# Kernel tuning notes

Measured on AMD Instinct MI355X. Metric: run time of the kernel, lower is better.

Reference implementation:

```python
import math
import jax, jax.numpy as jnp
import numpy as np
from jax import lax

# ---- static config (mirrors RPN init + typical torchvision anchor setup) ----
IMG_H = IMG_W = 800
LEVELS = [(200, 200, 4, 32), (100, 100, 8, 64), (50, 50, 16, 128), (25, 25, 32, 256), (13, 13, 64, 512)]  # (h, w, stride, anchor_size)
RATIOS = (0.5, 1.0, 2.0)
COUNTS = tuple(h * w * len(RATIOS) for (h, w, _, _) in LEVELS)  # (120000,30000,7500,1875,507)
A_TOTAL = sum(COUNTS)  # 159882
PRE_NMS = 2000
POST_NMS = 1000
NMS_THRESH = 0.7
MIN_SIZE = 1e-3
BBOX_CLIP = math.log(1000.0 / 16)


def make_anchors():
    parts = []
    for (h, w, stride, size) in LEVELS:
        ws = np.array([size * np.sqrt(1.0 / r) for r in RATIOS], np.float32)  # [3]
        hs = np.array([size * np.sqrt(r) for r in RATIOS], np.float32)
        sx = (np.arange(w, dtype=np.float32) + 0.5) * stride
        sy = (np.arange(h, dtype=np.float32) + 0.5) * stride
        cy, cx = np.meshgrid(sy, sx, indexing='ij')
        cx = cx.reshape(-1, 1)
        cy = cy.reshape(-1, 1)
        a = np.stack([cx - ws / 2, cy - hs / 2, cx + ws / 2, cy + hs / 2], axis=-1)  # [HW,3,4]
        parts.append(a.reshape(-1, 4))
    return np.concatenate(parts, 0).astype(np.float32)


def setup_inputs() -> dict:
    key = jax.random.key(0)
    k1, k2 = jax.random.split(key)
    scores = jax.random.normal(k1, (1, A_TOTAL), dtype=jnp.float32)
    deltas = jax.random.normal(k2, (A_TOTAL, 4), dtype=jnp.float32) * 0.5
    anchors = jnp.asarray(make_anchors())
    return {'scores': scores, 'deltas': deltas, 'anchors': anchors}


def _pairwise_iou(b):
    area = (b[:, 2] - b[:, 0]) * (b[:, 3] - b[:, 1])  # [K]
    lt = jnp.maximum(b[:, None, :2], b[None, :, :2])   # [K,K,2]
    rb = jnp.minimum(b[:, None, 2:], b[None, :, 2:])
    wh = jnp.maximum(rb - lt, 0.0)
    inter = wh[..., 0] * wh[..., 1]
    return inter / (area[:, None] + area[None, :] - inter)


def reference(scores, deltas, anchors):
    s_all = lax.stop_gradient(scores[0])  # original does cls.detach()
    # ---- box decode (torchvision-style) ----
    w = anchors[:, 2] - anchors[:, 0]
    h = anchors[:, 3] - anchors[:, 1]
    cx = anchors[:, 0] + 0.5 * w
    cy = anchors[:, 1] + 0.5 * h
    dx, dy = deltas[:, 0], deltas[:, 1]
    dw = jnp.minimum(deltas[:, 2], BBOX_CLIP)
    dh = jnp.minimum(deltas[:, 3], BBOX_CLIP)
    px = cx + dx * w
    py = cy + dy * h
    pw = jnp.exp(dw) * w
    ph = jnp.exp(dh) * h
    boxes = jnp.stack([px - 0.5 * pw, py - 0.5 * ph, px + 0.5 * pw, py + 0.5 * ph], axis=1)  # [A,4]
    # ---- per-level top-k over objectness ----
    idx_parts = []
    off = 0
    for c in COUNTS:
        k = min(PRE_NMS, c)
        _, ti = lax.top_k(lax.dynamic_slice_in_dim(s_all, off, c), k)
        idx_parts.append(ti + off)
        off += c
    top_idx = jnp.concatenate(idx_parts)  # [K=8382]
    K = top_idx.shape[0]
    s = s_all[top_idx]
    b = boxes[top_idx]
    # ---- clip to image + min-size validity (masked instead of compacted) ----
    b = jnp.stack([jnp.clip(b[:, 0], 0.0, IMG_W), jnp.clip(b[:, 1], 0.0, IMG_H),
                   jnp.clip(b[:, 2], 0.0, IMG_W), jnp.clip(b[:, 3], 0.0, IMG_H)], axis=1)
    valid = ((b[:, 2] - b[:, 0]) >= MIN_SIZE) & ((b[:, 3] - b[:, 1]) >= MIN_SIZE)
    # ---- per-level NMS offset; replicates original feature_mask[keep] indexing
    # (positional indexing into the full anchor-order level-id vector) ----
    fmask_full = np.concatenate([np.full(c, i, np.float32) for i, c in enumerate(COUNTS)])
    fmask = jnp.asarray(fmask_full[:K])
    box_max = jnp.max(jnp.where(valid[:, None], b, -jnp.inf))
    bn = b + (fmask * (box_max + 1.0))[:, None]
    # ---- greedy NMS on score-sorted candidates ----
    s_m = jnp.where(valid, s, -jnp.inf)
    order = jnp.argsort(-s_m)
    s_srt = s_m[order]
    b_srt = b[order]
    iou = _pairwise_iou(bn[order])  # [K,K] ~281MB
    ar = jnp.arange(K)

    def body(i, keep):
        sup = (iou[i] > NMS_THRESH) & (ar > i)
        return jnp.where(keep[i], keep & ~sup, keep)

    keep = lax.fori_loop(0, K, body, s_srt > -jnp.inf)
    final = jnp.where(keep, s_srt, -jnp.inf)
    out_s, oidx = lax.top_k(final, POST_NMS)  # top post_nms kept, score order; -inf pads
    out_b = b_srt[oidx]
    return out_b, out_s
```

## Files before the change

### kernel.cpp

```cpp
#include <hip/hip_runtime.h>
#include <math.h>

typedef unsigned int u32;
typedef unsigned long long u64;
typedef unsigned char u8;

#define K_TOT 8382
#define NCH 131
#define CAP 1024
#define EC 64
#define GCAP 32768
#define IMGSZ 800.0f

__device__ __constant__ int LOFF[5] = {0, 120000, 150000, 157500, 159375};
__device__ __constant__ int LCNT[5] = {120000, 30000, 7500, 1875, 507};
__device__ __constant__ int KSEL[5] = {2000, 2000, 2000, 1875, 507};
__device__ __constant__ int SELB[5] = {0, 2000, 4000, 6000, 7875};
__device__ __constant__ int HBS[4] = {0, 118, 148, 156};
__device__ __constant__ int GBS[6] = {0, 118, 148, 156, 158, 159};

static __device__ __forceinline__ u32 fkey(float x) {
    u32 u = __float_as_uint(x);
    u32 m = (u32)(((int)u) >> 31) | 0x80000000u;
    return u ^ m;
}

static __device__ __forceinline__ int lvl_of(int s) {
    return (s < 2000) ? 0 : (s < 4000) ? 1 : (s < 6000) ? 2 : (s < 7875) ? 3 : 4;
}

static __device__ __forceinline__ u32 rdl32(u32 v, int j) {
    return (u32)__builtin_amdgcn_readlane((int)v, j);
}
static __device__ __forceinline__ u64 rdlane64(u64 v, int j) {
    u32 lo = (u32)__builtin_amdgcn_readlane((int)(u32)v, j);
    u32 hi = (u32)__builtin_amdgcn_readlane((int)(u32)(v >> 32), j);
    return ((u64)hi << 32) | (u64)lo;
}

static __device__ __forceinline__ u32 wor32(u32 x) {
    x |= (u32)__builtin_amdgcn_update_dpp(0, (int)x, 0x111, 0xf, 0xf, true);
    x |= (u32)__builtin_amdgcn_update_dpp(0, (int)x, 0x112, 0xf, 0xf, true);
    x |= (u32)__builtin_amdgcn_update_dpp(0, (int)x, 0x114, 0xf, 0xf, true);
    x |= (u32)__builtin_amdgcn_update_dpp(0, (int)x, 0x118, 0xf, 0xf, true);
    x |= (u32)__builtin_amdgcn_update_dpp(0, (int)x, 0x142, 0xa, 0xf, true);
    x |= (u32)__builtin_amdgcn_update_dpp(0, (int)x, 0x143, 0xc, 0xf, true);
    return x;
}

static __device__ __forceinline__ void thresh_scan(const u32* hist, u32* scanbuf, int m,
                                                   u32 need, u32* sv, int t) {
    for (int i = t; i < m; i += 1024) scanbuf[i] = hist[m - 1 - i];
    __syncthreads();
    for (int ofs = 1; ofs < m; ofs <<= 1) {
        int i0 = t, i1 = t + 1024;
        u32 a0 = 0, a1 = 0;
        if (i0 < m && i0 >= ofs) a0 = scanbuf[i0 - ofs];
        if (i1 < m && i1 >= ofs) a1 = scanbuf[i1 - ofs];
        __syncthreads();
        if (i0 < m && i0 >= ofs) scanbuf[i0] += a0;
        if (i1 < m && i1 >= ofs) scanbuf[i1] += a1;
        __syncthreads();
    }
    for (int i = t; i < m; i += 1024) {
        u32 inc = scanbuf[i];
        u32 exc = i ? scanbuf[i - 1] : 0;
        if (inc >= need && exc < need) { sv[0] = (u32)(m - 1 - i); sv[1] = need - exc; }
    }
    __syncthreads();
}

__global__ __launch_bounds__(1024) void k_hist(const float* __restrict__ scores,
                                               u32* __restrict__ hist3) {
    __shared__ u32 lh[2048];
    int t = threadIdx.x;
    lh[t] = 0; lh[t + 1024] = 0;
    __syncthreads();
    int b = blockIdx.x;
    int l = (b < HBS[1]) ? 0 : (b < HBS[2]) ? 1 : 2;
    int i = (b - HBS[l]) * 1024 + t;
    if (i < LCNT[l]) atomicAdd(&lh[fkey(scores[LOFF[l] + i]) >> 21], 1u);
    __syncthreads();
    u32* h = hist3 + l * 2048;
    if (lh[t]) atomicAdd(&h[t], lh[t]);
    if (lh[t + 1024]) atomicAdd(&h[t + 1024], lh[t + 1024]);
}

__global__ __launch_bounds__(1024) void k_thresh(const u32* __restrict__ hist3,
                                                 u32* __restrict__ tinfo) {
    __shared__ u32 scanbuf[2048];
    __shared__ u32 sv[2];
    int l = blockIdx.x;
    int t = threadIdx.x;
    thresh_scan(hist3 + l * 2048, scanbuf, 2048, (u32)KSEL[l], sv, t);
    if (t == 0) { tinfo[l * 2] = sv[0]; tinfo[l * 2 + 1] = sv[1]; }
}

__global__ __launch_bounds__(1024) void k_gather(const float* __restrict__ scores,
                                                 const u32* __restrict__ tinfo,
                                                 u32* __restrict__ sel, u32* __restrict__ cgt,
                                                 u32* __restrict__ gcnt, u32* __restrict__ gidx,
                                                 u32* __restrict__ gkey) {
    int b = blockIdx.x;
    int l = (b < GBS[1]) ? 0 : (b < GBS[2]) ? 1 : (b < GBS[3]) ? 2 : (b < GBS[4]) ? 3 : 4;
    int i = (b - GBS[l]) * 1024 + threadIdx.x;
    if (i >= LCNT[l]) return;
    int off = LOFF[l], sb = SELB[l];
    if (l >= 3) { sel[sb + i] = (u32)(off + i); return; }
    u32 ky = fkey(scores[off + i]);
    u32 b1 = tinfo[l * 2];
    u32 top = ky >> 21;
    if (top > b1) {
        u32 p = atomicAdd(&cgt[l], 1u);
        sel[sb + p] = (u32)(off + i);
    } else if (top == b1) {
        u32 e = atomicAdd(&gcnt[l], 1u);
        if (e < GCAP) { gidx[l * GCAP + e] = (u32)i; gkey[l * GCAP + e] = ky; }
    }
}

__global__ __launch_bounds__(1024) void k_final(const u32* __restrict__ gidx,
                                                const u32* __restrict__ gkey,
                                                const u32* __restrict__ gcnt,
                                                const u32* __restrict__ tinfo,
                                                u32* __restrict__ sel) {
    __shared__ u32 hist[2048];
    __shared__ u32 scanbuf[2048];
    __shared__ u32 eqbuf[1024];
    __shared__ u32 sv[2];
    __shared__ u32 c2, ceq;
    int l = blockIdx.x;
    int t = threadIdx.x;
    int k = KSEL[l], sb = SELB[l], off = LOFF[l];
    u32 m = gcnt[l]; if (m > GCAP) m = GCAP;
    u32 b1 = tinfo[l * 2];
    u32 need = tinfo[l * 2 + 1];
    const u32* kb = gkey + l * GCAP;
    const u32* ib = gidx + l * GCAP;
    hist[t] = 0; hist[t + 1024] = 0; __syncthreads();
    for (u32 e = t; e < m; e += 1024) atomicAdd(&hist[(kb[e] >> 10) & 2047u], 1u);
    __syncthreads();
    thresh_scan(hist, scanbuf, 2048, need, sv, t);
    u32 b2 = sv[0], need2 = sv[1];
    __syncthreads();
    hist[t] = 0; __syncthreads();
    for (u32 e = t; e < m; e += 1024) {
        u32 ky = kb[e];
        if (((ky >> 10) & 2047u) == b2) atomicAdd(&hist[ky & 1023u], 1u);
    }
    __syncthreads();
    thresh_scan(hist, scanbuf, 1024, need2, sv, t);
    u32 T = (b1 << 21) | (b2 << 10) | sv[0];
    u32 take = sv[1];
    if (t == 0) { c2 = 0; ceq = 0; }
    __syncthreads();
    u32 nGTbin = need - take;
    u32 base2 = (u32)sb + (u32)k - need;
    for (u32 e = t; e < m; e += 1024) {
        u32 ky = kb[e];
        if (ky > T) { u32 p = atomicAdd(&c2, 1u); sel[base2 + p] = (u32)off + ib[e]; }
        else if (ky == T) { u32 q = atomicAdd(&ceq, 1u); if (q < 1024) eqbuf[q] = ib[e]; }
    }
    __syncthreads();
    if (t == 0) {
        int n = (ceq > 1024u) ? 1024 : (int)ceq;
        for (int a = 1; a < n; ++a) {
            u32 v = eqbuf[a]; int bq = a - 1;
            while (bq >= 0 && eqbuf[bq] > v) { eqbuf[bq + 1] = eqbuf[bq]; --bq; }
            eqbuf[bq + 1] = v;
        }
        for (u32 q = 0; q < take; ++q) sel[base2 + nGTbin + q] = (u32)off + eqbuf[q];
    }
}

__global__ void k_decode(const float* __restrict__ scores, const float4* __restrict__ deltas,
                         const float4* __restrict__ anchors, const u32* __restrict__ sel,
                         float4* __restrict__ candB, float* __restrict__ candS,
                         u32* __restrict__ candV, u32* __restrict__ candA) {
    int s = blockIdx.x * 256 + threadIdx.x;
    if (s >= K_TOT) return;
    u32 a = sel[s];
    float4 an = anchors[a];
    float4 dl = deltas[a];
    float sc = scores[a];
    float w = __fsub_rn(an.z, an.x), h = __fsub_rn(an.w, an.y);
    float cx = __fadd_rn(an.x, __fmul_rn(0.5f, w));
    float cy = __fadd_rn(an.y, __fmul_rn(0.5f, h));
    const float CLIPV = (float)4.1351665567423563;
    float dw = fminf(dl.z, CLIPV);
    float dh = fminf(dl.w, CLIPV);
    float px = __fadd_rn(cx, __fmul_rn(dl.x, w));
    float py = __fadd_rn(cy, __fmul_rn(dl.y, h));
    float pw = __fmul_rn((float)exp((double)dw), w);
    float ph = __fmul_rn((float)exp((double)dh), h);
    float x1 = __fsub_rn(px, __fmul_rn(0.5f, pw));
    float y1 = __fsub_rn(py, __fmul_rn(0.5f, ph));
    float x2 = __fadd_rn(px, __fmul_rn(0.5f, pw));
    float y2 = __fadd_rn(py, __fmul_rn(0.5f, ph));
    x1 = fminf(fmaxf(x1, 0.0f), IMGSZ);
    y1 = fminf(fmaxf(y1, 0.0f), IMGSZ);
    x2 = fminf(fmaxf(x2, 0.0f), IMGSZ);
    y2 = fminf(fmaxf(y2, 0.0f), IMGSZ);
    bool valid = (__fsub_rn(x2, x1) >= 0.001f) && (__fsub_rn(y2, y1) >= 0.001f);
    candB[s] = make_float4(x1, y1, x2, y2);
    candS[s] = sc;
    candV[s] = valid ? 1u : 0u;
    candA[s] = a;
}

__global__ __launch_bounds__(256) void k_rank_lvl(const float* __restrict__ candS,
                                                  const u32* __restrict__ candA,
                                                  u32* __restrict__ Praw) {
    __shared__ u64 tile[256];
    int l = blockIdx.z;
    int cnt = KSEL[l], base = SELB[l];
    int tx = blockIdx.x * 256;
    int ty = blockIdx.y * 256;
    if (tx >= cnt || ty >= cnt) return;
    int t = threadIdx.x;
    u64 Aj = ~0ull;
    if (tx + t < cnt) {
        int j = base + tx + t;
        Aj = ((u64)(~fkey(candS[j])) << 32) | (u64)candA[j];
    }
    tile[t] = Aj;
    __syncthreads();
    int si = ty + t;
    if (si >= cnt) return;
    int s = base + si;
    u64 A = ((u64)(~fkey(candS[s])) << 32) | (u64)candA[s];
    int r = 0;
#pragma unroll 8
    for (int q = 0; q < 256; ++q) r += (tile[q] < A);
    if (r) atomicAdd(&Praw[s], (u32)r);
}

__global__ __launch_bounds__(256) void k_rank_glob(const float* __restrict__ candS,
                                                   const u32* __restrict__ candV,
                                                   const u32* __restrict__ Praw,
                                                   u32* __restrict__ rank) {
    __shared__ u64 colB[256];
    int t = threadIdx.x;
    int cj = blockIdx.x * 256 + t;
    u64 B = ~0ull;
    if (cj < K_TOT) {
        u32 smk = candV[cj] ? fkey(candS[cj]) : 0x007FFFFFu;
        u32 Pj = (u32)SELB[lvl_of(cj)] + Praw[cj];
        B = ((u64)(~smk) << 32) | (u64)Pj;
    }
    colB[t] = B;
    __syncthreads();
    int s = blockIdx.y * 256 + t;
    if (s >= K_TOT) return;
    u32 smk = candV[s] ? fkey(candS[s]) : 0x007FFFFFu;
    u32 Ps = (u32)SELB[lvl_of(s)] + Praw[s];
    u64 myB = ((u64)(~smk) << 32) | (u64)Ps;
    int cnt = 0;
#pragma unroll 8
    for (int j = 0; j < 256; ++j) cnt += (colB[j] < myB);
    if (cnt) atomicAdd(&rank[s], (u32)cnt);
}

__global__ void k_scatter(const float4* __restrict__ candB, const float* __restrict__ candS,
                          const u32* __restrict__ candV, const u32* __restrict__ rank,
                          float4* __restrict__ sB, float* __restrict__ sArea,
                          float* __restrict__ sS, u32* __restrict__ sV) {
    int s = blockIdx.x * 256 + threadIdx.x;
    if (s >= K_TOT) return;
    u32 r = rank[s];
    float4 b = candB[s];
    float area = __fmul_rn(__fsub_rn(b.z, b.x), __fsub_rn(b.w, b.y));
    sB[r] = b; sArea[r] = area; sS[r] = candS[s]; sV[r] = candV[s];
}

__global__ __launch_bounds__(256) void k_mask(const float4* __restrict__ sB,
                                              const float* __restrict__ sArea,
                                              const u32* __restrict__ sV,
                                              u64* __restrict__ vwords,
                                              u64* __restrict__ diag, u32* __restrict__ ecnt,
                                              ulonglong2* __restrict__ epack,
                                              u64* __restrict__ dmask) {
    __shared__ float4 cb[64];
    __shared__ float ca[64];
    int wd = blockIdx.x;
    int t = threadIdx.x;
    if (t < 64) {
        int j = wd * 64 + t;
        if (j < K_TOT) { cb[t] = sB[j]; ca[t] = sArea[j]; }
        else { cb[t] = make_float4(0.f, 0.f, 0.f, 0.f); ca[t] = 0.f; }
    }
    __syncthreads();
    int i = blockIdx.y * 256 + t;
    if (i >= K_TOT) return;
    int dwr = i >> 6;
    if (wd < dwr) return;
    float4 bi = sB[i];
    float ai = sArea[i];
    u64 bits = 0;
    int jbase = wd * 64;
    for (int j2 = 0; j2 < 64; ++j2) {
        int j = jbase + j2;
        if (j > i && j < K_TOT) {
            float4 bj = cb[j2];
            float ltx = fmaxf(bi.x, bj.x), lty = fmaxf(bi.y, bj.y);
            float rbx = fminf(bi.z, bj.z), rby = fminf(bi.w, bj.w);
            float wx = fmaxf(__fsub_rn(rbx, ltx), 0.0f);
            float wy = fmaxf(__fsub_rn(rby, lty), 0.0f);
            float inter = __fmul_rn(wx, wy);
            if (inter > 0.0f) {
                float uni = __fsub_rn(__fadd_rn(ai, ca[j2]), inter);
                float iou = inter / uni;
                if (iou > 0.7f) bits |= (1ull << j2);
            }
        }
    }
    if (wd == dwr) {
        diag[i] = bits;
        u64 vb = __ballot(sV[i] != 0u);
        u64 db = __ballot(bits != 0ull);
        if ((i & 63) == 0) { vwords[wd] = vb; dmask[wd] = db; }
    } else if (bits != 0ull) {
        u32 p = atomicAdd(&ecnt[wd], 1u);
        if (p < CAP) epack[wd * CAP + p] = make_ulonglong2((u64)i, bits);
    }
}

__global__ __launch_bounds__(1024) void k_scan(const u64* __restrict__ diag,
                                               const u64* __restrict__ vwords,
                                               const u32* __restrict__ ecnt,
                                               const ulonglong2* __restrict__ tpack,
                                               const u64* __restrict__ dmask,
                                               const float4* __restrict__ sB,
                                               const float* __restrict__ sS,
                                               float* __restrict__ out) {
    __shared__ ulonglong2 sTpack[NCH * EC];
    __shared__ u64 sKeepArr[NCH];
    __shared__ u32 pc[NCH + 1];
    int t = threadIdx.x;
    int w = t >> 6, lane = t & 63;
    {
        int e0 = t, e1 = t + 1024, e2 = t + 2048, e3 = t + 3072, e4 = t + 4096;
        int e5 = t + 5120, e6 = t + 6144, e7 = t + 7168, e8 = t + 8192;
        bool p8 = e8 < NCH * EC;
        ulonglong2 a0 = tpack[(size_t)(e0 >> 6) * CAP + (e0 & 63)];
        ulonglong2 a1 = tpack[(size_t)(e1 >> 6) * CAP + (e1 & 63)];
        ulonglong2 a2 = tpack[(size_t)(e2 >> 6) * CAP + (e2 & 63)];
        ulonglong2 a3 = tpack[(size_t)(e3 >> 6) * CAP + (e3 & 63)];
        ulonglong2 a4 = tpack[(size_t)(e4 >> 6) * CAP + (e4 & 63)];
        ulonglong2 a5 = tpack[(size_t)(e5 >> 6) * CAP + (e5 & 63)];
        ulonglong2 a6 = tpack[(size_t)(e6 >> 6) * CAP + (e6 & 63)];
        ulonglong2 a7 = tpack[(size_t)(e7 >> 6) * CAP + (e7 & 63)];
        ulonglong2 a8 = make_ulonglong2(0ull, 0ull);
        if (p8) a8 = tpack[(size_t)(e8 >> 6) * CAP + (e8 & 63)];
        sTpack[e0] = a0; sTpack[e1] = a1; sTpack[e2] = a2; sTpack[e3] = a3;
        sTpack[e4] = a4; sTpack[e5] = a5; sTpack[e6] = a6; sTpack[e7] = a7;
        if (p8) sTpack[e8] = a8;
    }
    u64 v0 = 0, v1 = 0, v2 = 0, m0 = 0, m1 = 0, m2 = 0;
    u32 c0 = 0, c1 = 0, c2 = 0;
    if (w == 0) {
        int i0 = lane, i1 = lane + 64, i2 = lane + 128;
        bool p2 = (i2 < NCH);
        v0 = vwords[i0]; v1 = vwords[i1]; v2 = p2 ? vwords[i2] : 0;
        c0 = ecnt[i0]; c1 = ecnt[i1]; c2 = p2 ? ecnt[i2] : 0;
        m0 = dmask[i0]; m1 = dmask[i1]; m2 = p2 ? dmask[i2] : 0;
        if (c0 > CAP) c0 = CAP;
        if (c1 > CAP) c1 = CAP;
        if (c2 > CAP) c2 = CAP;
    }
    __syncthreads();
    if (w == 0) {
        ulonglong2 Ea = sTpack[EC + lane];
        u64 Dcur = diag[lane];
        u64 Dnx  = diag[64 + lane];
        u64 vw = rdlane64(v0, 0), dmw = rdlane64(m0, 0);
        u64 inc = 0;
        u32 cntn = rdl32(c0, 1);
        for (int c = 0; c < NCH; ++c) {
            int cn  = (c + 1 < NCH) ? (c + 1) : c;
            int cn2 = (c + 2 < NCH) ? (c + 2) : c;
            ulonglong2 Eb = sTpack[cn2 * EC + lane];
            u64 Dnn = diag[cn2 * 64 + lane];
            u32 sidx = (u32)Ea.x;
            u32 sch = sidx >> 6;
            u64 Kw = sKeepArr[(sch < (u32)NCH) ? sch : 0];
            u32 cntn2; u64 vwn, dmn;
            if (cn < 64)       { vwn = rdlane64(v0, cn);       dmn = rdlane64(m0, cn); }
            else if (cn < 128) { vwn = rdlane64(v1, cn - 64);  dmn = rdlane64(m1, cn - 64); }
            else               { vwn = rdlane64(v2, cn - 128); dmn = rdlane64(m2, cn - 128); }
            if (cn2 < 64)       cntn2 = rdl32(c0, cn2);
            else if (cn2 < 128) cntn2 = rdl32(c1, cn2 - 64);
            else                cntn2 = rdl32(c2, cn2 - 128);
            u64 alive = vw & ~inc;
            if (dmw) {
                u64 dm = dmw & alive;
                while (dm) {
                    int j = __builtin_ctzll(dm);
                    dm &= dm - 1;
                    if ((alive >> j) & 1ull) {
                        alive &= ~rdlane64(Dcur, j);
                        dm &= alive;
                    }
                }
            }
            if (lane == 0) sKeepArr[c] = alive;
            u64 m = 0;
            if ((u32)lane < cntn) {
                u64 kw2 = (sch == (u32)c) ? alive : Kw;
                if ((kw2 >> (sidx & 63u)) & 1ull) m = Ea.y;
            }
            u32 lo = wor32((u32)m);
            u32 hi = wor32((u32)(m >> 32));
            u64 incn = ((u64)rdl32(hi, 63) << 32) | (u64)rdl32(lo, 63);
            if (cntn > (u32)EC) {
                u64 mt = 0;
                for (u32 e = (u32)EC + (u32)lane; e < cntn; e += 64u) {
                    ulonglong2 Et = tpack[(size_t)cn * CAP + e];
                    u32 si = (u32)Et.x;
                    u32 sc2 = si >> 6;
                    u64 kw3 = (sc2 == (u32)c) ? alive : sKeepArr[sc2];
                    if ((kw3 >> (si & 63u)) & 1ull) mt |= Et.y;
                }
                lo = wor32((u32)mt);
                hi = wor32((u32)(mt >> 32));
                incn |= ((u64)rdl32(hi, 63) << 32) | (u64)rdl32(lo, 63);
            }
            inc = incn;
            Ea = Eb; Dcur = Dnx; Dnx = Dnn;
            vw = vwn; dmw = dmn; cntn = cntn2;
        }
    }
    __syncthreads();
    if (t < NCH) pc[t + 1] = (u32)__popcll(sKeepArr[t]);
    if (t == 0) pc[0] = 0;
    __syncthreads();
    for (int ofs = 1; ofs < NCH; ofs <<= 1) {
        int i = t + 1;
        u32 v = 0;
        bool p = (t < NCH) && (i - ofs >= 1);
        if (p) v = pc[i - ofs];
        __syncthreads();
        if (p) pc[i] += v;
        __syncthreads();
    }
    u32 nk = pc[NCH];
    for (int i = t; i < K_TOT; i += 1024) {
        int wi = i >> 6, b = i & 63;
        u64 kw = sKeepArr[wi];
        u32 kb = pc[wi] + (u32)__popcll(kw & ((1ull << b) - 1ull));
        bool kp = (kw >> b) & 1ull;
        if (kp) {
            if (kb < 1000u) {
                float4 bx = sB[i];
                out[kb * 4 + 0] = bx.x; out[kb * 4 + 1] = bx.y;
                out[kb * 4 + 2] = bx.z; out[kb * 4 + 3] = bx.w;
                out[4000 + kb] = sS[i];
            }
        } else {
            u32 q = (u32)i - kb;
            u32 slot = nk + q;
            if (slot < 1000u) {
                float4 bx = sB[i];
                out[slot * 4 + 0] = bx.x; out[slot * 4 + 1] = bx.y;
                out[slot * 4 + 2] = bx.z; out[slot * 4 + 3] = bx.w;
                out[4000 + slot] = -INFINITY;
            }
        }
    }
}

static constexpr size_t al256(size_t x) { return (x + 255) & ~(size_t)255; }
static constexpr size_t KB4 = (size_t)K_TOT * 4;
static constexpr size_t KB16 = (size_t)K_TOT * 16;
static constexpr size_t O_RANK = 0;
static constexpr size_t O_PRAW = al256(O_RANK + KB4);
static constexpr size_t O_ECNT = al256(O_PRAW + KB4);
static constexpr size_t O_HIST = al256(O_ECNT + (size_t)NCH * 4);
static constexpr size_t O_CGT = al256(O_HIST + (size_t)3 * 2048 * 4);
static constexpr size_t O_GCNT = al256(O_CGT + 3 * 4);
static constexpr size_t MEMSET_BYTES = al256(O_GCNT + 3 * 4);
static constexpr size_t O_TINFO = MEMSET_BYTES;
static constexpr size_t O_SEL = al256(O_TINFO + 6 * 4);
static constexpr size_t O_GIDX = al256(O_SEL + KB4);
static constexpr size_t O_GKEY = al256(O_GIDX + (size_t)3 * GCAP * 4);
static constexpr size_t O_CANDB = al256(O_GKEY + (size_t)3 * GCAP * 4);
static constexpr size_t O_CANDS = al256(O_CANDB + KB16);
static constexpr size_t O_CANDV = al256(O_CANDS + KB4);
static constexpr size_t O_CANDA = al256(O_CANDV + KB4);
static constexpr size_t O_SB = al256(O_CANDA + KB4);
static constexpr size_t O_SAREA = al256(O_SB + KB16);
static constexpr size_t O_SS = al256(O_SAREA + KB4);
static constexpr size_t O_SV = al256(O_SS + KB4);
static constexpr size_t O_VW = al256(O_SV + KB4);
static constexpr size_t O_DMASK = al256(O_VW + (size_t)NCH * 8);
static constexpr size_t O_DIAG = al256(O_DMASK + (size_t)NCH * 8);
static constexpr size_t O_EPACK = al256(O_DIAG + (size_t)(NCH * 64) * 8);

extern "C" void kernel_launch(void* const* d_in, const int* in_sizes, int n_in,
                              void* d_out, int out_size, void* d_ws, size_t ws_size,
                              hipStream_t stream) {
    const float* scores = (const float*)d_in[0];
    const float4* deltas = (const float4*)d_in[1];
    const float4* anchors = (const float4*)d_in[2];
    float* out = (float*)d_out;
    char* ws = (char*)d_ws;

    u32* rank = (u32*)(ws + O_RANK);
    u32* Praw = (u32*)(ws + O_PRAW);
    u32* ecnt = (u32*)(ws + O_ECNT);
    u32* hist3 = (u32*)(ws + O_HIST);
    u32* cgt = (u32*)(ws + O_CGT);
    u32* gcnt = (u32*)(ws + O_GCNT);
    u32* tinfo = (u32*)(ws + O_TINFO);
    u32* sel = (u32*)(ws + O_SEL);
    u32* gidx = (u32*)(ws + O_GIDX);
    u32* gkey = (u32*)(ws + O_GKEY);
    float4* candB = (float4*)(ws + O_CANDB);
    float* candS = (float*)(ws + O_CANDS);
    u32* candV = (u32*)(ws + O_CANDV);
    u32* candA = (u32*)(ws + O_CANDA);
    float4* sB = (float4*)(ws + O_SB);
    float* sArea = (float*)(ws + O_SAREA);
    float* sS = (float*)(ws + O_SS);
    u32* sV = (u32*)(ws + O_SV);
    u64* vwords = (u64*)(ws + O_VW);
    u64* dmask = (u64*)(ws + O_DMASK);
    u64* diag = (u64*)(ws + O_DIAG);
    ulonglong2* epack = (ulonglong2*)(ws + O_EPACK);

    hipMemsetAsync(ws, 0, MEMSET_BYTES, stream);

    const int NBLK = (K_TOT + 255) / 256;
    k_hist<<<156, 1024, 0, stream>>>(scores, hist3);
    k_thresh<<<3, 1024, 0, stream>>>(hist3, tinfo);
    k_gather<<<159, 1024, 0, stream>>>(scores, tinfo, sel, cgt, gcnt, gidx, gkey);
    k_final<<<3, 1024, 0, stream>>>(gidx, gkey, gcnt, tinfo, sel);
    k_decode<<<NBLK, 256, 0, stream>>>(scores, deltas, anchors, sel, candB, candS, candV, candA);
    k_rank_lvl<<<dim3(8, 8, 5), 256, 0, stream>>>(candS, candA, Praw);
    k_rank_glob<<<dim3(NBLK, NBLK), 256, 0, stream>>>(candS, candV, Praw, rank);
    k_scatter<<<NBLK, 256, 0, stream>>>(candB, candS, candV, rank, sB, sArea, sS, sV);
    k_mask<<<dim3(NCH, NBLK), 256, 0, stream>>>(sB, sArea, sV, vwords, diag, ecnt, epack, dmask);
    k_scan<<<1, 1024, 0, stream>>>(diag, vwords, ecnt, epack, dmask, sB, sS, out);
}
```

Before: 212.9 us.

## Distribute NMS chunk scan across all warps with progress-flag dataflow

Replaces the single-wave sequential chunk scan, which staged edge packs in shared memory and prefetched, with a scheme where each of the 16 waves owns chunks round-robin. A wave resolves incoming suppression edges as soon as their source chunk's keep word is published, tracked through a workgroup-scope atomic progress counter with acquire/release ordering. It then finishes its own chunk and publishes. This overlaps the edge gathering and loads of later chunks with the serial chain, at the cost of spin-polling shared memory and a longer per-chunk critical path through the atomic handoff between waves.

Result: no change. 210.3 us (-1.2%).

```diff
diff --git a/kernel.cpp b/kernel.cpp
--- a/kernel.cpp
+++ b/kernel.cpp
@@ -8,7 +8,6 @@
 #define K_TOT 8382
 #define NCH 131
 #define CAP 1024
-#define EC 64
 #define GCAP 32768
 #define IMGSZ 800.0f
 
@@ -333,101 +332,69 @@
                                                const float4* __restrict__ sB,
                                                const float* __restrict__ sS,
                                                float* __restrict__ out) {
-    __shared__ ulonglong2 sTpack[NCH * EC];
     __shared__ u64 sKeepArr[NCH];
     __shared__ u32 pc[NCH + 1];
+    __shared__ u32 sProg;
     int t = threadIdx.x;
     int w = t >> 6, lane = t & 63;
-    {
-        int e0 = t, e1 = t + 1024, e2 = t + 2048, e3 = t + 3072, e4 = t + 4096;
-        int e5 = t + 5120, e6 = t + 6144, e7 = t + 7168, e8 = t + 8192;
-        bool p8 = e8 < NCH * EC;
-        ulonglong2 a0 = tpack[(size_t)(e0 >> 6) * CAP + (e0 & 63)];
-        ulonglong2 a1 = tpack[(size_t)(e1 >> 6) * CAP + (e1 & 63)];
-        ulonglong2 a2 = tpack[(size_t)(e2 >> 6) * CAP + (e2 & 63)];
-        ulonglong2 a3 = tpack[(size_t)(e3 >> 6) * CAP + (e3 & 63)];
-        ulonglong2 a4 = tpack[(size_t)(e4 >> 6) * CAP + (e4 & 63)];
-        ulonglong2 a5 = tpack[(size_t)(e5 >> 6) * CAP + (e5 & 63)];
-        ulonglong2 a6 = tpack[(size_t)(e6 >> 6) * CAP + (e6 & 63)];
-        ulonglong2 a7 = tpack[(size_t)(e7 >> 6) * CAP + (e7 & 63)];
-        ulonglong2 a8 = make_ulonglong2(0ull, 0ull);
-        if (p8) a8 = tpack[(size_t)(e8 >> 6) * CAP + (e8 & 63)];
-        sTpack[e0] = a0; sTpack[e1] = a1; sTpack[e2] = a2; sTpack[e3] = a3;
-        sTpack[e4] = a4; sTpack[e5] = a5; sTpack[e6] = a6; sTpack[e7] = a7;
-        if (p8) sTpack[e8] = a8;
-    }
-    u64 v0 = 0, v1 = 0, v2 = 0, m0 = 0, m1 = 0, m2 = 0;
-    u32 c0 = 0, c1 = 0, c2 = 0;
-    if (w == 0) {
-        int i0 = lane, i1 = lane + 64, i2 = lane + 128;
-        bool p2 = (i2 < NCH);
-        v0 = vwords[i0]; v1 = vwords[i1]; v2 = p2 ? vwords[i2] : 0;
-        c0 = ecnt[i0]; c1 = ecnt[i1]; c2 = p2 ? ecnt[i2] : 0;
-        m0 = dmask[i0]; m1 = dmask[i1]; m2 = p2 ? dmask[i2] : 0;
-        if (c0 > CAP) c0 = CAP;
-        if (c1 > CAP) c1 = CAP;
-        if (c2 > CAP) c2 = CAP;
-    }
-    __syncthreads();
-    if (w == 0) {
-        ulonglong2 Ea = sTpack[EC + lane];
-        u64 Dcur = diag[lane];
-        u64 Dnx  = diag[64 + lane];
-        u64 vw = rdlane64(v0, 0), dmw = rdlane64(m0, 0);
+    if (t == 0) sProg = 0;
+    __syncthreads();
+    for (int c = w; c < NCH; c += 16) {
+        ulonglong2 E1 = tpack[(size_t)c * CAP + lane];
+        ulonglong2 E2 = tpack[(size_t)c * CAP + 64 + lane];
+        u64 Dc = diag[c * 64 + lane];
+        u64 vw = vwords[c];
+        u64 dmw = dmask[c];
+        u32 cnt = ecnt[c]; if (cnt > CAP) cnt = CAP;
+        u32 s1 = (u32)E1.x, s2 = (u32)E2.x;
+        u32 sch1 = s1 >> 6, sch2 = s2 >> 6;
+        u64 mbits = 0;
+        bool done1 = ((u32)lane >= cnt);
+        bool done2 = ((u32)(lane + 64) >= cnt);
+        if (c > 0) {
+            for (;;) {
+                u32 p = __hip_atomic_load(&sProg, __ATOMIC_ACQUIRE, __HIP_MEMORY_SCOPE_WORKGROUP);
+                if (!done1 && sch1 < p) {
+                    u64 kw = sKeepArr[sch1];
+                    if ((kw >> (s1 & 63u)) & 1ull) mbits |= E1.y;
+                    done1 = true;
+                }
+                if (!done2 && sch2 < p) {
+                    u64 kw = sKeepArr[sch2];
+                    if ((kw >> (s2 & 63u)) & 1ull) mbits |= E2.y;
+                    done2 = true;
+                }
+                if (p >= (u32)c) break;
+            }
+        }
         u64 inc = 0;
-        u32 cntn = rdl32(c0, 1);
-        for (int c = 0; c < NCH; ++c) {
-            int cn  = (c + 1 < NCH) ? (c + 1) : c;
-            int cn2 = (c + 2 < NCH) ? (c + 2) : c;
-            ulonglong2 Eb = sTpack[cn2 * EC + lane];
-            u64 Dnn = diag[cn2 * 64 + lane];
-            u32 sidx = (u32)Ea.x;
-            u32 sch = sidx >> 6;
-            u64 Kw = sKeepArr[(sch < (u32)NCH) ? sch : 0];
-            u32 cntn2; u64 vwn, dmn;
-            if (cn < 64)       { vwn = rdlane64(v0, cn);       dmn = rdlane64(m0, cn); }
-            else if (cn < 128) { vwn = rdlane64(v1, cn - 64);  dmn = rdlane64(m1, cn - 64); }
-            else               { vwn = rdlane64(v2, cn - 128); dmn = rdlane64(m2, cn - 128); }
-            if (cn2 < 64)       cntn2 = rdl32(c0, cn2);
-            else if (cn2 < 128) cntn2 = rdl32(c1, cn2 - 64);
-            else                cntn2 = rdl32(c2, cn2 - 128);
-            u64 alive = vw & ~inc;
-            if (dmw) {
-                u64 dm = dmw & alive;
-                while (dm) {
-                    int j = __builtin_ctzll(dm);
-                    dm &= dm - 1;
-                    if ((alive >> j) & 1ull) {
-                        alive &= ~rdlane64(Dcur, j);
-                        dm &= alive;
-                    }
+        if (cnt) {
+            if (cnt > 128u) {
+                for (u32 e = 128u + (u32)lane; e < cnt; e += 64u) {
+                    ulonglong2 Et = tpack[(size_t)c * CAP + e];
+                    u32 si = (u32)Et.x;
+                    if ((sKeepArr[si >> 6] >> (si & 63u)) & 1ull) mbits |= Et.y;
                 }
             }
-            if (lane == 0) sKeepArr[c] = alive;
-            u64 m = 0;
-            if ((u32)lane < cntn) {
-                u64 kw2 = (sch == (u32)c) ? alive : Kw;
-                if ((kw2 >> (sidx & 63u)) & 1ull) m = Ea.y;
+            u32 lo = wor32((u32)mbits);
+            u32 hi = wor32((u32)(mbits >> 32));
+            inc = ((u64)rdl32(hi, 63) << 32) | (u64)rdl32(lo, 63);
+        }
+        u64 alive = vw & ~inc;
+        if (dmw) {
+            u64 dm = dmw & alive;
+            while (dm) {
+                int j = __builtin_ctzll(dm);
+                dm &= dm - 1;
+                if ((alive >> j) & 1ull) {
+                    alive &= ~rdlane64(Dc, j);
+                    dm &= alive;
+                }
             }
-            u32 lo = wor32((u32)m);
-            u32 hi = wor32((u32)(m >> 32));
-            u64 incn = ((u64)rdl32(hi, 63) << 32) | (u64)rdl32(lo, 63);
-            if (cntn > (u32)EC) {
-                u64 mt = 0;
-                for (u32 e = (u32)EC + (u32)lane; e < cntn; e += 64u) {
-                    ulonglong2 Et = tpack[(size_t)cn * CAP + e];
-                    u32 si = (u32)Et.x;
-                    u32 sc2 = si >> 6;
-                    u64 kw3 = (sc2 == (u32)c) ? alive : sKeepArr[sc2];
-                    if ((kw3 >> (si & 63u)) & 1ull) mt |= Et.y;
-                }
-                lo = wor32((u32)mt);
-                hi = wor32((u32)(mt >> 32));
-                incn |= ((u64)rdl32(hi, 63) << 32) | (u64)rdl32(lo, 63);
-            }
-            inc = incn;
-            Ea = Eb; Dcur = Dnx; Dnx = Dnn;
-            vw = vwn; dmw = dmn; cntn = cntn2;
+        }
+        if (lane == 0) {
+            sKeepArr[c] = alive;
+            __hip_atomic_store(&sProg, (u32)(c + 1), __ATOMIC_RELEASE, __HIP_MEMORY_SCOPE_WORKGROUP);
         }
     }
     __syncthreads();
```
